# Kernel optimization log

Measured on AMD Instinct MI355X. Metric: run time of the kernel, lower is better.

The kernel has to match this reference:

```python
import jax, jax.numpy as jnp
import numpy as np

N = 51200      # total nodes
E = 1638400    # total edges (avg degree 32)
G = 512        # graphs in batch
IN = 16        # input node features
H = 4          # heads
C = 32         # channels per head
HC = H * C     # 128, concat output width
SLOPE = 0.2    # LeakyReLU negative slope
BN_EPS = 1e-5


def _glorot(k, shape, fan):
    return jax.random.normal(k, shape, jnp.float32) / np.sqrt(fan).astype(np.float32)


def setup_inputs() -> dict:
    key = jax.random.key(0)
    ks = jax.random.split(key, 32)
    inp = {}
    inp['x'] = jax.random.normal(ks[0], (N, IN), jnp.float32)
    inp['edge_index'] = jax.random.randint(ks[1], (2, E), 0, N)
    inp['batch'] = jnp.sort(jax.random.randint(ks[2], (N,), 0, G))
    # GATv2 layer 1 (IN -> H*C)
    inp['l1_Wl'] = _glorot(ks[3], (IN, HC), IN)
    inp['l1_bl'] = jnp.zeros((HC,), jnp.float32)
    inp['l1_Wr'] = _glorot(ks[4], (IN, HC), IN)
    inp['l1_br'] = jnp.zeros((HC,), jnp.float32)
    inp['l1_att'] = _glorot(ks[5], (H, C), C)
    inp['l1_bias'] = jnp.zeros((HC,), jnp.float32)
    # GATv2 layer 2 (HC -> H*C)
    inp['l2_Wl'] = _glorot(ks[6], (HC, HC), HC)
    inp['l2_bl'] = jnp.zeros((HC,), jnp.float32)
    inp['l2_Wr'] = _glorot(ks[7], (HC, HC), HC)
    inp['l2_br'] = jnp.zeros((HC,), jnp.float32)
    inp['l2_att'] = _glorot(ks[8], (H, C), C)
    inp['l2_bias'] = jnp.zeros((HC,), jnp.float32)
    # MLP head (HC -> HC -> HC -> 2) with BatchNorm (eval mode, running stats 0/1)
    inp['fc1_W'] = _glorot(ks[9], (HC, HC), HC)
    inp['fc1_b'] = jnp.zeros((HC,), jnp.float32)
    inp['bn1_g'] = jnp.ones((HC,), jnp.float32)
    inp['bn1_b'] = jnp.zeros((HC,), jnp.float32)
    inp['fc2_W'] = _glorot(ks[10], (HC, HC), HC)
    inp['fc2_b'] = jnp.zeros((HC,), jnp.float32)
    inp['bn2_g'] = jnp.ones((HC,), jnp.float32)
    inp['bn2_b'] = jnp.zeros((HC,), jnp.float32)
    inp['fc3_W'] = _glorot(ks[11], (HC, 2), HC)
    inp['fc3_b'] = jnp.zeros((2,), jnp.float32)
    return inp


def gatv2_conv(x, src, dst, Wl, bl, Wr, br, att, bias):
    # PyG GATv2Conv (share_weights=False, concat=True), eval mode (no dropout).
    xl = (x @ Wl + bl).reshape(-1, H, C)  # source transform  [N,H,C]
    xr = (x @ Wr + br).reshape(-1, H, C)  # target transform  [N,H,C]
    e = jax.nn.leaky_relu(xl[src] + xr[dst], SLOPE)   # [E,H,C]
    score = jnp.einsum('ehc,hc->eh', e, att)          # [E,H]
    # segment softmax over edges sharing the same target node
    m = jax.ops.segment_max(score, dst, num_segments=N)
    ex = jnp.exp(score - m[dst])
    denom = jax.ops.segment_sum(ex, dst, num_segments=N)
    alpha = ex / (denom[dst] + 1e-16)                 # [E,H]
    out = jax.ops.segment_sum(xl[src] * alpha[:, :, None], dst, num_segments=N)
    return out.reshape(-1, HC) + bias


def reference(x, edge_index, batch,
              l1_Wl, l1_bl, l1_Wr, l1_br, l1_att, l1_bias,
              l2_Wl, l2_bl, l2_Wr, l2_br, l2_att, l2_bias,
              fc1_W, fc1_b, bn1_g, bn1_b,
              fc2_W, fc2_b, bn2_g, bn2_b,
              fc3_W, fc3_b):
    src, dst = edge_index[0], edge_index[1]
    h = jax.nn.relu(gatv2_conv(x, src, dst, l1_Wl, l1_bl, l1_Wr, l1_br, l1_att, l1_bias))
    h = jax.nn.relu(gatv2_conv(h, src, dst, l2_Wl, l2_bl, l2_Wr, l2_br, l2_att, l2_bias))
    # global mean pool over graphs
    s = jax.ops.segment_sum(h, batch, num_segments=G)
    cnt = jax.ops.segment_sum(jnp.ones((N,), h.dtype), batch, num_segments=G)
    g = s / jnp.maximum(cnt, 1.0)[:, None]            # [G,HC]
    # MLP head; BatchNorm1d in eval mode with running_mean=0, running_var=1
    def bn(z, gamma, beta):
        return z * (gamma / np.sqrt(1.0 + BN_EPS).astype(np.float32)) + beta
    g = jax.nn.relu(bn(g @ fc1_W + fc1_b, bn1_g, bn1_b))
    g = jax.nn.relu(bn(g @ fc2_W + fc2_b, bn2_g, bn2_b))
    return g @ fc3_W + fc3_b                          # [G,2]
```

## Files before the change

### kernel.cpp

```cpp
#include <hip/hip_runtime.h>
#include <math.h>

#define NN 51200
#define EE 1638400
#define GG 512
#define INF 16
#define HCC 128
#define NB 400
#define TILE 4096

typedef float vf2 __attribute__((ext_vector_type(2)));
#define FMA2 __builtin_elementwise_fma
#define MIN2 __builtin_elementwise_min
#define MAX2 __builtin_elementwise_max


__device__ __forceinline__ int wave_incl_scan(int v, int lane) {
#pragma unroll
    for (int d = 1; d < 64; d <<= 1) {
        int y = __shfl_up(v, d);
        if (lane >= d) v += y;
    }
    return v;
}

__global__ __launch_bounds__(256) void k_hist(const int* __restrict__ ei,
                                              int* __restrict__ bcnt) {
    __shared__ int h[NB];
    for (int i = threadIdx.x; i < NB; i += 256) h[i] = 0;
    __syncthreads();
    int e0 = blockIdx.x * TILE;
#pragma unroll
    for (int s = 0; s < 16; s++) {
        int d = ei[EE + e0 + s * 256 + threadIdx.x];
        atomicAdd(&h[d >> 7], 1);
    }
    __syncthreads();
    for (int i = threadIdx.x; i < NB; i += 256)
        if (h[i]) atomicAdd(&bcnt[i], h[i]);
}

__global__ __launch_bounds__(512) void k_scan2(const int* __restrict__ bcnt,
                                               int* __restrict__ bbase,
                                               int* __restrict__ gcur,
                                               int* __restrict__ rowptr) {
    __shared__ int sc[512];
    int t = threadIdx.x;
    int v = (t < NB) ? bcnt[t] : 0;
    sc[t] = v;
    __syncthreads();
    for (int off = 1; off < 512; off <<= 1) {
        int u = (t >= off) ? sc[t - off] : 0;
        __syncthreads();
        sc[t] += u;
        __syncthreads();
    }
    if (t < NB) { int ex = sc[t] - v; bbase[t] = ex; gcur[t] = ex; }
    if (t == 0) { bbase[NB] = EE; rowptr[NN] = EE; }
}

__global__ __launch_bounds__(512) void k_bin(const int* __restrict__ ei,
                                             int* __restrict__ gcur,
                                             unsigned* __restrict__ binned) {
    __shared__ int h[512];
    __shared__ int lexcl[NB], lcur[NB], baseg[NB];
    __shared__ unsigned stage[TILE];
    __shared__ int wsum[8];
    int t = threadIdx.x;
    int lane = t & 63, w = t >> 6;
    h[t] = 0;
    __syncthreads();
    int e0 = blockIdx.x * TILE;
    int sv[8], dv[8];
#pragma unroll
    for (int s = 0; s < 8; s++) {
        int e = e0 + s * 512 + t;
        sv[s] = ei[e];
        dv[s] = ei[EE + e];
        atomicAdd(&h[dv[s] >> 7], 1);
    }
    __syncthreads();
    int myh = h[t];
    int incl = wave_incl_scan(myh, lane);
    if (lane == 63) wsum[w] = incl;
    __syncthreads();
    int woff = 0;
    for (int i = 0; i < w; i++) woff += wsum[i];
    incl += woff;
    if (t < NB) {
        int ex = incl - myh;
        lexcl[t] = ex;
        lcur[t] = ex;
        baseg[t] = atomicAdd(&gcur[t], myh);
    }
    __syncthreads();
#pragma unroll
    for (int s = 0; s < 8; s++) {
        int b = dv[s] >> 7;
        int r = atomicAdd(&lcur[b], 1);
        stage[r] = (unsigned)sv[s] | ((unsigned)dv[s] << 16);
    }
    __syncthreads();
#pragma unroll
    for (int s = 0; s < 8; s++) {
        int idx = s * 512 + t;
        unsigned p = stage[idx];
        int b = (int)(p >> 23);
        binned[baseg[b] + idx - lexcl[b]] = p;
    }
}

__global__ __launch_bounds__(256) void k_csr(const unsigned* __restrict__ binned,
                                             const int* __restrict__ bbase,
                                             int* __restrict__ rowptr,
                                             int* __restrict__ col) {
    int b = blockIdx.x;
    int base = bbase[b];
    int cnt = bbase[b + 1] - base;
    __shared__ int nh[1024], ncur[1024];
    __shared__ int wsum[4];
    int t = threadIdx.x;
    int lane = t & 63, w = t >> 6;
#pragma unroll
    for (int i = 0; i < 4; i++) nh[t + 256 * i] = 0;
    __syncthreads();
    for (int e = t; e < cnt; e += 256) {
        unsigned p = binned[base + e];
        unsigned src = p & 0xFFFFu;
        int key = (int)(((p >> 16) & 127u) << 3) | (int)(src >> 13);
        atomicAdd(&nh[key], 1);
    }
    __syncthreads();
    int c0 = nh[4 * t + 0], c1 = nh[4 * t + 1], c2 = nh[4 * t + 2], c3 = nh[4 * t + 3];
    int tot = ((c0 + c1) + (c2 + c3));
    int incl = wave_incl_scan(tot, lane);
    if (lane == 63) wsum[w] = incl;
    __syncthreads();
    int woff = 0;
    for (int i = 0; i < w; i++) woff += wsum[i];
    int tex = incl + woff - tot;
    ncur[4 * t + 0] = base + tex;
    ncur[4 * t + 1] = base + tex + c0;
    ncur[4 * t + 2] = base + tex + c0 + c1;
    ncur[4 * t + 3] = base + tex + c0 + c1 + c2;
    if ((t & 1) == 0) rowptr[(b << 7) + (t >> 1)] = base + tex;
    __syncthreads();
    for (int e = t; e < cnt; e += 256) {
        unsigned p = binned[base + e];
        unsigned src = p & 0xFFFFu;
        int key = (int)(((p >> 16) & 127u) << 3) | (int)(src >> 13);
        int r = atomicAdd(&ncur[key], 1);
        col[r] = (int)src;
    }
}

__global__ __launch_bounds__(256) void k_lin1(const float* __restrict__ x,
                                              const float* __restrict__ Wl,
                                              const float* __restrict__ bl,
                                              const float* __restrict__ Wr,
                                              const float* __restrict__ br,
                                              float* __restrict__ xl,
                                              float* __restrict__ xr) {
    __shared__ float sx[2][INF];
    int j = threadIdx.x & 127;
    int ty = threadIdx.x >> 7;
    int row = blockIdx.x * 2 + ty;
    if (threadIdx.x < 32) {
        int r = blockIdx.x * 2 + (threadIdx.x >> 4);
        sx[threadIdx.x >> 4][threadIdx.x & 15] = x[(size_t)r * INF + (threadIdx.x & 15)];
    }
    __syncthreads();
    float al = bl[j], ar = br[j];
#pragma unroll
    for (int k = 0; k < INF; k++) {
        float xv = sx[ty][k];
        al = fmaf(xv, Wl[k * HCC + j], al);
        ar = fmaf(xv, Wr[k * HCC + j], ar);
    }
    int s = 64 * ((j >> 2) & 1) + 4 * (j >> 3) + (j & 3);
    xl[(size_t)row * HCC + s] = al;
    xr[(size_t)row * HCC + s] = ar;
}

#define AST 129
#define BST 260
__global__ __launch_bounds__(512) void k_lin2(const float* __restrict__ hin,
                                              const float* __restrict__ Wl,
                                              const float* __restrict__ bl,
                                              const float* __restrict__ Wr,
                                              const float* __restrict__ br,
                                              float* __restrict__ outl,
                                              float* __restrict__ outr) {
    __shared__ float As[32 * AST];
    __shared__ float Bs[32 * BST];
    const int tid = threadIdx.x;
    const int cx = tid & 31;
    const int cy = tid >> 5;
    const int r0 = blockIdx.x * 128;

    float accL[8][4], accR[8][4];
#pragma unroll
    for (int j = 0; j < 8; j++)
#pragma unroll
        for (int i = 0; i < 4; i++) { accL[j][i] = 0.f; accR[j][i] = 0.f; }

    for (int k0 = 0; k0 < HCC; k0 += 32) {
#pragma unroll
        for (int s = 0; s < 2; s++) {
            int f = tid + 512 * s;
            int row = f >> 3;
            int kk = (f & 7) * 4;
            float4 v = *(const float4*)(hin + (size_t)(r0 + row) * HCC + k0 + kk);
            As[(kk + 0) * AST + row] = v.x;
            As[(kk + 1) * AST + row] = v.y;
            As[(kk + 2) * AST + row] = v.z;
            As[(kk + 3) * AST + row] = v.w;
        }
#pragma unroll
        for (int s = 0; s < 4; s++) {
            int g = tid + 512 * s;
            int kr = g >> 6;
            int c4 = g & 63;
            const float* srcp = (c4 < 32)
                ? (Wl + (size_t)(k0 + kr) * HCC + c4 * 4)
                : (Wr + (size_t)(k0 + kr) * HCC + (c4 - 32) * 4);
            *(float4*)&Bs[kr * BST + c4 * 4] = *(const float4*)srcp;
        }
        __syncthreads();
#pragma unroll 4
        for (int k = 0; k < 32; ++k) {
            float a[8];
#pragma unroll
            for (int j = 0; j < 8; ++j) a[j] = As[k * AST + cy + 16 * j];
            float4 b4l = *(const float4*)&Bs[k * BST + cx * 4];
            float4 b4r = *(const float4*)&Bs[k * BST + 128 + cx * 4];
#pragma unroll
            for (int j = 0; j < 8; ++j) {
                accL[j][0] = fmaf(a[j], b4l.x, accL[j][0]);
                accL[j][1] = fmaf(a[j], b4l.y, accL[j][1]);
                accL[j][2] = fmaf(a[j], b4l.z, accL[j][2]);
                accL[j][3] = fmaf(a[j], b4l.w, accL[j][3]);
                accR[j][0] = fmaf(a[j], b4r.x, accR[j][0]);
                accR[j][1] = fmaf(a[j], b4r.y, accR[j][1]);
                accR[j][2] = fmaf(a[j], b4r.z, accR[j][2]);
                accR[j][3] = fmaf(a[j], b4r.w, accR[j][3]);
            }
        }
        __syncthreads();
    }
    float4 bv_l = *(const float4*)(bl + cx * 4);
    float4 bv_r = *(const float4*)(br + cx * 4);
    const int soff = 64 * (cx & 1) + (cx >> 1) * 4;
#pragma unroll
    for (int j = 0; j < 8; ++j) {
        int row = r0 + cy + 16 * j;
        float4 o;
        o.x = accL[j][0] + bv_l.x;
        o.y = accL[j][1] + bv_l.y;
        o.z = accL[j][2] + bv_l.z;
        o.w = accL[j][3] + bv_l.w;
        *(float4*)(outl + (size_t)row * HCC + soff) = o;
        o.x = accR[j][0] + bv_r.x;
        o.y = accR[j][1] + bv_r.y;
        o.z = accR[j][2] + bv_r.z;
        o.w = accR[j][3] + bv_r.w;
        *(float4*)(outr + (size_t)row * HCC + soff) = o;
    }
}

__global__ __launch_bounds__(256) void k_attn(const int* __restrict__ rowptr,
                                              const int* __restrict__ col,
                                              const float* __restrict__ xl,
                                              const float* __restrict__ xr,
                                              const float* __restrict__ att,
                                              const float* __restrict__ bias,
                                              float* __restrict__ hout) {
    const int wave = threadIdx.x >> 6;
    const int lane = threadIdx.x & 63;
    const int sub = lane >> 4;
    const int q = lane & 15;
    const int n = blockIdx.x * 4 + wave;

    const float4 xrv0 = *(const float4*)(xr + (size_t)n * HCC + q * 4);
    const float4 xrv1 = *(const float4*)(xr + (size_t)n * HCC + 64 + q * 4);
    const float4 at0 = *(const float4*)(att + q * 8);
    const float4 at1 = *(const float4*)(att + q * 8 + 4);
    const vf2 xr01 = {xrv0.x, xrv0.y}, xr23 = {xrv0.z, xrv0.w};
    const vf2 xr45 = {xrv1.x, xrv1.y}, xr67 = {xrv1.z, xrv1.w};
    const vf2 at01 = {at0.x, at0.y}, at23 = {at0.z, at0.w};
    const vf2 at45 = {at1.x, at1.y}, at67 = {at1.z, at1.w};
    const vf2 Z2 = {0.f, 0.f}, C2 = {0.2f, 0.2f};
    const unsigned choff = (unsigned)q * 16u;

    const int base = rowptr[n];
    const int deg = rowptr[n + 1] - base;

    float m = -INFINITY, l = 0.f;
    vf2 a01 = Z2, a23 = Z2, a45 = Z2, a67 = Z2;

    for (int i0 = 0; i0 < deg; i0 += 64) {
        int mye = 0;
        if (i0 + lane < deg) mye = col[base + i0 + lane];
        const int cnt = min(64, deg - i0);
        const int groups = (cnt + 15) >> 4;
        for (int g = 0; g < groups; ++g) {
            vf2 v01[4], v23[4], v45[4], v67[4];
#pragma unroll
            for (int k = 0; k < 4; ++k) {
                const int src = __shfl(mye, 16 * g + 4 * k + sub);
                const unsigned voff = ((unsigned)src << 9) + choff;
                const float4 v0 = *(const float4*)((const char*)xl + voff);
                const float4 v1 = *(const float4*)((const char*)xl + voff + 256);
                v01[k] = (vf2){v0.x, v0.y}; v23[k] = (vf2){v0.z, v0.w};
                v45[k] = (vf2){v1.x, v1.y}; v67[k] = (vf2){v1.z, v1.w};
            }
            float p[4];
#pragma unroll
            for (int k = 0; k < 4; ++k) {
                vf2 e, kk, p2;
                e = v01[k] + xr01; kk = FMA2(C2, MIN2(e, Z2), MAX2(e, Z2)); p2 = kk * at01;
                e = v23[k] + xr23; kk = FMA2(C2, MIN2(e, Z2), MAX2(e, Z2)); p2 = FMA2(kk, at23, p2);
                e = v45[k] + xr45; kk = FMA2(C2, MIN2(e, Z2), MAX2(e, Z2)); p2 = FMA2(kk, at45, p2);
                e = v67[k] + xr67; kk = FMA2(C2, MIN2(e, Z2), MAX2(e, Z2)); p2 = FMA2(kk, at67, p2);
                float pp = p2.x + p2.y;
                pp += __shfl_xor(pp, 1);
                pp += __shfl_xor(pp, 2);
                if ((16 * g + 4 * k + sub) >= cnt) pp = -INFINITY;
                p[k] = pp;
            }
            float pm = fmaxf(fmaxf(p[0], p[1]), fmaxf(p[2], p[3]));
            pm = fmaxf(pm, __shfl_xor(pm, 16));
            pm = fmaxf(pm, __shfl_xor(pm, 32));
            const float mn = fmaxf(m, pm);
            const float sc = __expf(m - mn);
            const float w0 = __expf(p[0] - mn);
            const float w1 = __expf(p[1] - mn);
            const float w2 = __expf(p[2] - mn);
            const float w3 = __expf(p[3] - mn);
            l = fmaf(l, sc, (w0 + w1) + (w2 + w3));
            const vf2 S = {sc, sc};
            const vf2 W0 = {w0, w0}, W1 = {w1, w1}, W2 = {w2, w2}, W3 = {w3, w3};
            a01 = FMA2(W3, v01[3], FMA2(W2, v01[2], FMA2(W1, v01[1], FMA2(W0, v01[0], a01 * S))));
            a23 = FMA2(W3, v23[3], FMA2(W2, v23[2], FMA2(W1, v23[1], FMA2(W0, v23[0], a23 * S))));
            a45 = FMA2(W3, v45[3], FMA2(W2, v45[2], FMA2(W1, v45[1], FMA2(W0, v45[0], a45 * S))));
            a67 = FMA2(W3, v67[3], FMA2(W2, v67[2], FMA2(W1, v67[1], FMA2(W0, v67[0], a67 * S))));
            m = mn;
        }
    }
    l += __shfl_xor(l, 16);
    l += __shfl_xor(l, 32);
    float af[8] = {a01.x, a01.y, a23.x, a23.y, a45.x, a45.y, a67.x, a67.y};
#pragma unroll
    for (int i = 0; i < 8; i++) {
        af[i] += __shfl_xor(af[i], 16);
        af[i] += __shfl_xor(af[i], 32);
    }
    const float inv = 1.f / (l + 1e-16f);
    if (sub == 0) {
        const float4 b0 = *(const float4*)(bias + q * 8);
        const float4 b1 = *(const float4*)(bias + q * 8 + 4);
        float4 o0, o1;
        o0.x = fmaxf(fmaf(af[0], inv, b0.x), 0.f);
        o0.y = fmaxf(fmaf(af[1], inv, b0.y), 0.f);
        o0.z = fmaxf(fmaf(af[2], inv, b0.z), 0.f);
        o0.w = fmaxf(fmaf(af[3], inv, b0.w), 0.f);
        o1.x = fmaxf(fmaf(af[4], inv, b1.x), 0.f);
        o1.y = fmaxf(fmaf(af[5], inv, b1.y), 0.f);
        o1.z = fmaxf(fmaf(af[6], inv, b1.z), 0.f);
        o1.w = fmaxf(fmaf(af[7], inv, b1.w), 0.f);
        *(float4*)(hout + (size_t)n * HCC + q * 8) = o0;
        *(float4*)(hout + (size_t)n * HCC + q * 8 + 4) = o1;
    }
}

__global__ __launch_bounds__(128) void k_head(const float* __restrict__ h,
                                              const int* __restrict__ batch,
                                              const float* __restrict__ fc1W, const float* __restrict__ fc1b,
                                              const float* __restrict__ bn1g, const float* __restrict__ bn1b,
                                              const float* __restrict__ fc2W, const float* __restrict__ fc2b,
                                              const float* __restrict__ bn2g, const float* __restrict__ bn2b,
                                              const float* __restrict__ fc3W, const float* __restrict__ fc3b,
                                              float* __restrict__ out) {
    int g = blockIdx.x;
    int j = threadIdx.x;
    __shared__ float buf[HCC], buf2[HCC];
    int lo = 0, hi = NN;
    while (lo < hi) { int mid = (lo + hi) >> 1; if (batch[mid] < g) lo = mid + 1; else hi = mid; }
    int s = lo;
    lo = 0; hi = NN;
    while (lo < hi) { int mid = (lo + hi) >> 1; if (batch[mid] < g + 1) lo = mid + 1; else hi = mid; }
    int e = lo;
    float s0 = 0.f, s1 = 0.f, s2 = 0.f, s3 = 0.f;
    int n = s;
    for (; n + 3 < e; n += 4) {
        s0 += h[(size_t)n * HCC + j];
        s1 += h[(size_t)(n + 1) * HCC + j];
        s2 += h[(size_t)(n + 2) * HCC + j];
        s3 += h[(size_t)(n + 3) * HCC + j];
    }
    for (; n < e; n++) s0 += h[(size_t)n * HCC + j];
    float sum = (s0 + s1) + (s2 + s3);
    float cnt = (float)(e - s);
    buf[j] = sum / fmaxf(cnt, 1.0f);
    __syncthreads();
    const float SQ = 1.00000499998749994f;
    float a = fc1b[j];
    for (int k = 0; k < HCC; k++) a = fmaf(buf[k], fc1W[k * HCC + j], a);
    a = fmaf(a, bn1g[j] / SQ, bn1b[j]);
    a = fmaxf(a, 0.f);
    buf2[j] = a;
    __syncthreads();
    a = fc2b[j];
    for (int k = 0; k < HCC; k++) a = fmaf(buf2[k], fc2W[k * HCC + j], a);
    a = fmaf(a, bn2g[j] / SQ, bn2b[j]);
    a = fmaxf(a, 0.f);
    buf[j] = a;
    __syncthreads();
    if (j < 2) {
        float o = fc3b[j];
        for (int k = 0; k < HCC; k++) o = fmaf(buf[k], fc3W[k * 2 + j], o);
        out[g * 2 + j] = o;
    }
}

extern "C" void kernel_launch(void* const* d_in, const int* in_sizes, int n_in,
                              void* d_out, int out_size, void* d_ws, size_t ws_size,
                              hipStream_t stream) {
    const float* x      = (const float*)d_in[0];
    const int*   ei     = (const int*)d_in[1];
    const int*   batch  = (const int*)d_in[2];
    const float* l1_Wl  = (const float*)d_in[3];
    const float* l1_bl  = (const float*)d_in[4];
    const float* l1_Wr  = (const float*)d_in[5];
    const float* l1_br  = (const float*)d_in[6];
    const float* l1_att = (const float*)d_in[7];
    const float* l1_bias= (const float*)d_in[8];
    const float* l2_Wl  = (const float*)d_in[9];
    const float* l2_bl  = (const float*)d_in[10];
    const float* l2_Wr  = (const float*)d_in[11];
    const float* l2_br  = (const float*)d_in[12];
    const float* l2_att = (const float*)d_in[13];
    const float* l2_bias= (const float*)d_in[14];
    const float* fc1_W  = (const float*)d_in[15];
    const float* fc1_b  = (const float*)d_in[16];
    const float* bn1_g  = (const float*)d_in[17];
    const float* bn1_b  = (const float*)d_in[18];
    const float* fc2_W  = (const float*)d_in[19];
    const float* fc2_b  = (const float*)d_in[20];
    const float* bn2_g  = (const float*)d_in[21];
    const float* bn2_b  = (const float*)d_in[22];
    const float* fc3_W  = (const float*)d_in[23];
    const float* fc3_b  = (const float*)d_in[24];
    float* out = (float*)d_out;

    float* xl = (float*)d_ws;
    float* xr = xl + (size_t)NN * HCC;
    float* h  = xr + (size_t)NN * HCC;
    int* rowptr = (int*)(h + (size_t)NN * HCC);
    int* col    = rowptr + (NN + 1);
    int* bcnt   = col + EE;
    int* bbase  = bcnt + NB;
    int* gcur   = bbase + (NB + 1);
    unsigned* binned = (unsigned*)xl;

    hipMemsetAsync(bcnt, 0, NB * sizeof(int), stream);
    k_hist<<<EE / TILE, 256, 0, stream>>>(ei, bcnt);
    k_scan2<<<1, 512, 0, stream>>>(bcnt, bbase, gcur, rowptr);
    k_bin<<<EE / TILE, 512, 0, stream>>>(ei, gcur, binned);
    k_csr<<<NB, 256, 0, stream>>>(binned, bbase, rowptr, col);

    k_lin1<<<NN / 2, 256, 0, stream>>>(x, l1_Wl, l1_bl, l1_Wr, l1_br, xl, xr);
    k_attn<<<NN / 4, 256, 0, stream>>>(rowptr, col, xl, xr, l1_att, l1_bias, h);

    k_lin2<<<NN / 128, 512, 0, stream>>>(h, l2_Wl, l2_bl, l2_Wr, l2_br, xl, xr);
    k_attn<<<NN / 4, 256, 0, stream>>>(rowptr, col, xl, xr, l2_att, l2_bias, h);

    k_head<<<GG, 128, 0, stream>>>(h, batch, fc1_W, fc1_b, bn1_g, bn1_b,
                                   fc2_W, fc2_b, bn2_g, bn2_b, fc3_W, fc3_b, out);
}
```

Before: 490.5 us.

## Store xl/xr head-major and split attention kernel per head

The linear kernels now write xl/xr as four head planes of [N,32] instead of node-major interleaved rows. The attention kernel launches one grid slice per head, so each wave gathers 128-byte source rows from a single 6.5 MB plane rather than 512-byte rows from the full array. The aim is a gather working set that fits better in cache and fewer registers per thread, which should raise occupancy. The cost is that col and rowptr are read four times, and the per-edge softmax bookkeeping (shuffles, exps) is repeated for each head.

```diff
diff --git a/kernel.cpp b/kernel.cpp
--- a/kernel.cpp
+++ b/kernel.cpp
@@ -8,6 +8,7 @@
 #define HCC 128
 #define NB 400
 #define TILE 4096
+#define NBLK (NN / 4)
 
 typedef float vf2 __attribute__((ext_vector_type(2)));
 #define FMA2 __builtin_elementwise_fma
@@ -177,9 +178,9 @@
         al = fmaf(xv, Wl[k * HCC + j], al);
         ar = fmaf(xv, Wr[k * HCC + j], ar);
     }
-    int s = 64 * ((j >> 2) & 1) + 4 * (j >> 3) + (j & 3);
-    xl[(size_t)row * HCC + s] = al;
-    xr[(size_t)row * HCC + s] = ar;
+    size_t s = ((size_t)(j >> 5) * NN + row) * 32 + (j & 31);
+    xl[s] = al;
+    xr[s] = ar;
 }
 
 #define AST 129
@@ -250,7 +251,8 @@
     }
     float4 bv_l = *(const float4*)(bl + cx * 4);
     float4 bv_r = *(const float4*)(br + cx * 4);
-    const int soff = 64 * (cx & 1) + (cx >> 1) * 4;
+    const size_t plane = (size_t)(cx >> 3) * NN * 32;
+    const int off = (cx & 7) * 4;
 #pragma unroll
     for (int j = 0; j < 8; ++j) {
         int row = r0 + cy + 16 * j;
@@ -259,12 +261,12 @@
         o.y = accL[j][1] + bv_l.y;
         o.z = accL[j][2] + bv_l.z;
         o.w = accL[j][3] + bv_l.w;
-        *(float4*)(outl + (size_t)row * HCC + soff) = o;
+        *(float4*)(outl + plane + (size_t)row * 32 + off) = o;
         o.x = accR[j][0] + bv_r.x;
         o.y = accR[j][1] + bv_r.y;
         o.z = accR[j][2] + bv_r.z;
         o.w = accR[j][3] + bv_r.w;
-        *(float4*)(outr + (size_t)row * HCC + soff) = o;
+        *(float4*)(outr + plane + (size_t)row * 32 + off) = o;
     }
 }
 
@@ -277,18 +279,16 @@
                                               float* __restrict__ hout) {
     const int wave = threadIdx.x >> 6;
     const int lane = threadIdx.x & 63;
-    const int sub = lane >> 4;
-    const int q = lane & 15;
-    const int n = blockIdx.x * 4 + wave;
-
-    const float4 xrv0 = *(const float4*)(xr + (size_t)n * HCC + q * 4);
-    const float4 xrv1 = *(const float4*)(xr + (size_t)n * HCC + 64 + q * 4);
-    const float4 at0 = *(const float4*)(att + q * 8);
-    const float4 at1 = *(const float4*)(att + q * 8 + 4);
-    const vf2 xr01 = {xrv0.x, xrv0.y}, xr23 = {xrv0.z, xrv0.w};
-    const vf2 xr45 = {xrv1.x, xrv1.y}, xr67 = {xrv1.z, xrv1.w};
-    const vf2 at01 = {at0.x, at0.y}, at23 = {at0.z, at0.w};
-    const vf2 at45 = {at1.x, at1.y}, at67 = {at1.z, at1.w};
+    const int sub = lane >> 3;
+    const int q = lane & 7;
+    const int head = blockIdx.x / NBLK;
+    const int n = (blockIdx.x - head * NBLK) * 4 + wave;
+
+    const float* xlh = xl + (size_t)head * NN * 32;
+    const float4 xrv = *(const float4*)(xr + ((size_t)head * NN + n) * 32 + q * 4);
+    const float4 atv = *(const float4*)(att + head * 32 + q * 4);
+    const vf2 xr01 = {xrv.x, xrv.y}, xr23 = {xrv.z, xrv.w};
+    const vf2 at01 = {atv.x, atv.y}, at23 = {atv.z, atv.w};
     const vf2 Z2 = {0.f, 0.f}, C2 = {0.2f, 0.2f};
     const unsigned choff = (unsigned)q * 16u;
 
@@ -296,7 +296,7 @@
     const int deg = rowptr[n + 1] - base;
 
     float m = -INFINITY, l = 0.f;
-    vf2 a01 = Z2, a23 = Z2, a45 = Z2, a67 = Z2;
+    vf2 a01 = Z2, a23 = Z2;
 
     for (int i0 = 0; i0 < deg; i0 += 64) {
         int mye = 0;
@@ -304,72 +304,63 @@
         const int cnt = min(64, deg - i0);
         const int groups = (cnt + 15) >> 4;
         for (int g = 0; g < groups; ++g) {
-            vf2 v01[4], v23[4], v45[4], v67[4];
-#pragma unroll
-            for (int k = 0; k < 4; ++k) {
-                const int src = __shfl(mye, 16 * g + 4 * k + sub);
-                const unsigned voff = ((unsigned)src << 9) + choff;
-                const float4 v0 = *(const float4*)((const char*)xl + voff);
-                const float4 v1 = *(const float4*)((const char*)xl + voff + 256);
-                v01[k] = (vf2){v0.x, v0.y}; v23[k] = (vf2){v0.z, v0.w};
-                v45[k] = (vf2){v1.x, v1.y}; v67[k] = (vf2){v1.z, v1.w};
+            float4 v[2];
+            float p[2];
+#pragma unroll
+            for (int k = 0; k < 2; ++k) {
+                const int src = __shfl(mye, 16 * g + 8 * k + sub);
+                const unsigned voff = ((unsigned)src << 7) + choff;
+                v[k] = *(const float4*)((const char*)xlh + voff);
             }
-            float p[4];
-#pragma unroll
-            for (int k = 0; k < 4; ++k) {
+#pragma unroll
+            for (int k = 0; k < 2; ++k) {
+                const vf2 v01 = {v[k].x, v[k].y}, v23 = {v[k].z, v[k].w};
                 vf2 e, kk, p2;
-                e = v01[k] + xr01; kk = FMA2(C2, MIN2(e, Z2), MAX2(e, Z2)); p2 = kk * at01;
-                e = v23[k] + xr23; kk = FMA2(C2, MIN2(e, Z2), MAX2(e, Z2)); p2 = FMA2(kk, at23, p2);
-                e = v45[k] + xr45; kk = FMA2(C2, MIN2(e, Z2), MAX2(e, Z2)); p2 = FMA2(kk, at45, p2);
-                e = v67[k] + xr67; kk = FMA2(C2, MIN2(e, Z2), MAX2(e, Z2)); p2 = FMA2(kk, at67, p2);
+                e = v01 + xr01; kk = FMA2(C2, MIN2(e, Z2), MAX2(e, Z2)); p2 = kk * at01;
+                e = v23 + xr23; kk = FMA2(C2, MIN2(e, Z2), MAX2(e, Z2)); p2 = FMA2(kk, at23, p2);
                 float pp = p2.x + p2.y;
                 pp += __shfl_xor(pp, 1);
                 pp += __shfl_xor(pp, 2);
-                if ((16 * g + 4 * k + sub) >= cnt) pp = -INFINITY;
+                pp += __shfl_xor(pp, 4);
+                if ((16 * g + 8 * k + sub) >= cnt) pp = -INFINITY;
                 p[k] = pp;
             }
-            float pm = fmaxf(fmaxf(p[0], p[1]), fmaxf(p[2], p[3]));
+            float pm = fmaxf(p[0], p[1]);
+            pm = fmaxf(pm, __shfl_xor(pm, 8));
             pm = fmaxf(pm, __shfl_xor(pm, 16));
             pm = fmaxf(pm, __shfl_xor(pm, 32));
             const float mn = fmaxf(m, pm);
             const float sc = __expf(m - mn);
             const float w0 = __expf(p[0] - mn);
             const float w1 = __expf(p[1] - mn);
-            const float w2 = __expf(p[2] - mn);
-            const float w3 = __expf(p[3] - mn);
-            l = fmaf(l, sc, (w0 + w1) + (w2 + w3));
-            const vf2 S = {sc, sc};
-            const vf2 W0 = {w0, w0}, W1 = {w1, w1}, W2 = {w2, w2}, W3 = {w3, w3};
-            a01 = FMA2(W3, v01[3], FMA2(W2, v01[2], FMA2(W1, v01[1], FMA2(W0, v01[0], a01 * S))));
-            a23 = FMA2(W3, v23[3], FMA2(W2, v23[2], FMA2(W1, v23[1], FMA2(W0, v23[0], a23 * S))));
-            a45 = FMA2(W3, v45[3], FMA2(W2, v45[2], FMA2(W1, v45[1], FMA2(W0, v45[0], a45 * S))));
-            a67 = FMA2(W3, v67[3], FMA2(W2, v67[2], FMA2(W1, v67[1], FMA2(W0, v67[0], a67 * S))));
+            l = fmaf(l, sc, w0 + w1);
+            const vf2 S = {sc, sc}, W0 = {w0, w0}, W1 = {w1, w1};
+            const vf2 v0_01 = {v[0].x, v[0].y}, v0_23 = {v[0].z, v[0].w};
+            const vf2 v1_01 = {v[1].x, v[1].y}, v1_23 = {v[1].z, v[1].w};
+            a01 = FMA2(W1, v1_01, FMA2(W0, v0_01, a01 * S));
+            a23 = FMA2(W1, v1_23, FMA2(W0, v0_23, a23 * S));
             m = mn;
         }
     }
+    l += __shfl_xor(l, 8);
     l += __shfl_xor(l, 16);
     l += __shfl_xor(l, 32);
-    float af[8] = {a01.x, a01.y, a23.x, a23.y, a45.x, a45.y, a67.x, a67.y};
-#pragma unroll
-    for (int i = 0; i < 8; i++) {
+    float af[4] = {a01.x, a01.y, a23.x, a23.y};
+#pragma unroll
+    for (int i = 0; i < 4; i++) {
+        af[i] += __shfl_xor(af[i], 8);
         af[i] += __shfl_xor(af[i], 16);
         af[i] += __shfl_xor(af[i], 32);
     }
     const float inv = 1.f / (l + 1e-16f);
     if (sub == 0) {
-        const float4 b0 = *(const float4*)(bias + q * 8);
-        const float4 b1 = *(const float4*)(bias + q * 8 + 4);
-        float4 o0, o1;
-        o0.x = fmaxf(fmaf(af[0], inv, b0.x), 0.f);
-        o0.y = fmaxf(fmaf(af[1], inv, b0.y), 0.f);
-        o0.z = fmaxf(fmaf(af[2], inv, b0.z), 0.f);
-        o0.w = fmaxf(fmaf(af[3], inv, b0.w), 0.f);
-        o1.x = fmaxf(fmaf(af[4], inv, b1.x), 0.f);
-        o1.y = fmaxf(fmaf(af[5], inv, b1.y), 0.f);
-        o1.z = fmaxf(fmaf(af[6], inv, b1.z), 0.f);
-        o1.w = fmaxf(fmaf(af[7], inv, b1.w), 0.f);
-        *(float4*)(hout + (size_t)n * HCC + q * 8) = o0;
-        *(float4*)(hout + (size_t)n * HCC + q * 8 + 4) = o1;
+        const float4 bv = *(const float4*)(bias + head * 32 + q * 4);
+        float4 o;
+        o.x = fmaxf(fmaf(af[0], inv, bv.x), 0.f);
+        o.y = fmaxf(fmaf(af[1], inv, bv.y), 0.f);
+        o.z = fmaxf(fmaf(af[2], inv, bv.z), 0.f);
+        o.w = fmaxf(fmaf(af[3], inv, bv.w), 0.f);
+        *(float4*)(hout + (size_t)n * HCC + head * 32 + q * 4) = o;
     }
 }
 
@@ -470,10 +461,10 @@
     k_csr<<<NB, 256, 0, stream>>>(binned, bbase, rowptr, col);
 
     k_lin1<<<NN / 2, 256, 0, stream>>>(x, l1_Wl, l1_bl, l1_Wr, l1_br, xl, xr);
-    k_attn<<<NN / 4, 256, 0, stream>>>(rowptr, col, xl, xr, l1_att, l1_bias, h);
+    k_attn<<<4 * NBLK, 256, 0, stream>>>(rowptr, col, xl, xr, l1_att, l1_bias, h);
 
     k_lin2<<<NN / 128, 512, 0, stream>>>(h, l2_Wl, l2_bl, l2_Wr, l2_br, xl, xr);
-    k_attn<<<NN / 4, 256, 0, stream>>>(rowptr, col, xl, xr, l2_att, l2_bias, h);
+    k_attn<<<4 * NBLK, 256, 0, stream>>>(rowptr, col, xl, xr, l2_att, l2_bias, h);
 
     k_head<<<GG, 128, 0, stream>>>(h, batch, fc1_W, fc1_b, bn1_g, bn1_b,
                                    fc2_W, fc2_b, bn2_g, bn2_b, fc3_W, fc3_b, out);
```

Measured after the change: 516.6 us. 1.05x slower.
